# Kernel tuning notes

Measured on AMD Instinct MI355X. Metric: run time of the kernel, lower is better.

Reference implementation:

```python
import jax, jax.numpy as jnp
import numpy as np
from jax import lax

B, T, D_IN, D_H, D_OUT = 64, 512, 256, 1024, 256


def setup_inputs() -> dict:
    key = jax.random.key(0)
    k1, k2, k3, k4 = jax.random.split(key, 4)
    # lecun_normal-style scaling: std = 1/sqrt(fan_in)
    inputs = jax.random.normal(k1, (B, T, D_IN), dtype=jnp.float32)
    input_kernel = jax.random.normal(k2, (D_IN, D_H), dtype=jnp.float32) / np.sqrt(D_IN)
    hidden_kernel = jax.random.normal(k3, (D_H, D_H), dtype=jnp.float32) / np.sqrt(D_H)
    hidden_bias = jnp.zeros((D_H,), dtype=jnp.float32)
    output_kernel = jax.random.normal(k4, (D_H, D_OUT), dtype=jnp.float32) / np.sqrt(D_H)
    output_bias = jnp.zeros((D_OUT,), dtype=jnp.float32)
    return {
        "inputs": inputs,
        "input_kernel": input_kernel,
        "hidden_kernel": hidden_kernel,
        "hidden_bias": hidden_bias,
        "output_kernel": output_kernel,
        "output_bias": output_bias,
    }


def reference(inputs, input_kernel, hidden_kernel, hidden_bias, output_kernel, output_bias):
    # inputs: [B, T, D_in]. Precompute the input projection for all timesteps
    # (batched GEMM) — same math as per-step x_t @ W_in inside scan.
    x_proj = jnp.einsum("bti,ih->bth", inputs, input_kernel) + hidden_bias  # [B,T,H]
    x_proj_tm = jnp.swapaxes(x_proj, 0, 1)  # time-major [T,B,H]

    def step(h, xp_t):
        h_new = jnp.tanh(xp_t + jnp.dot(h, hidden_kernel))  # [B,H]
        return h_new, h_new

    h0 = jnp.zeros((inputs.shape[0], hidden_kernel.shape[0]), dtype=inputs.dtype)
    _, hidden_states = lax.scan(step, h0, x_proj_tm)  # [T,B,H]
    hidden_states = jnp.swapaxes(hidden_states, 0, 1)  # [B,T,H]
    # Dense readout applied to every timestep (return_sequences=True)
    outputs = jnp.einsum("bth,ho->bto", hidden_states, output_kernel) + output_bias
    return outputs
```

## Files before the change

### kernel.cpp

```cpp
#include <hip/hip_runtime.h>
#include <stdint.h>
#include <stddef.h>


#define TT 512
#define HH 1024

typedef __attribute__((ext_vector_type(8))) short short8;
typedef __attribute__((ext_vector_type(4))) float f32x4;
typedef unsigned long long u64;

#define POISON 0xAAAAAAAAAAAAAAAAull

__device__ inline short f2bf(float f) {
  uint32_t u = __builtin_bit_cast(uint32_t, f);
  u += 0x7fffu + ((u >> 16) & 1u);
  return (short)(u >> 16);
}

__device__ inline float fast_tanh(float x) {
  float ax = fabsf(x);
  float e = __expf(-2.f * ax);
  float r = (1.f - e) * __builtin_amdgcn_rcpf(1.f + e);
  return copysignf(r, x);
}

__global__ __launch_bounds__(256, 1) void xproj_kernel(
    const float* __restrict__ inp,
    const float* __restrict__ w_in,
    const float* __restrict__ h_b,
    float* __restrict__ xp) {
  const int blk = blockIdx.x;
  const int c = blk & 3, s = blk >> 2;
  const int tid = threadIdx.x;
  const int wv = tid >> 6, l = tid & 63, lr = l & 15, lq = l >> 4;

  __shared__ short ldsA[16 * 264];

  short8 wf[8][4];
#pragma unroll
  for (int kt = 0; kt < 8; ++kt)
#pragma unroll
    for (int nt = 0; nt < 4; ++nt) {
      int col = c * 256 + (wv * 4 + nt) * 16 + lr;
      int k0 = kt * 32 + lq * 8;
      short8 v;
#pragma unroll
      for (int e = 0; e < 8; ++e) v[e] = f2bf(w_in[(size_t)(k0 + e) * HH + col]);
      wf[kt][nt] = v;
    }
  float bias[4];
#pragma unroll
  for (int nt = 0; nt < 4; ++nt) bias[nt] = h_b[c * 256 + (wv * 4 + nt) * 16 + lr];

  for (int it = 0; it < 32; ++it) {
    int m = s + 64 * it;
    int t = m >> 2, g = m & 3;
    {
      int row = tid >> 4, cb = (tid & 15) * 16;
      const float* src = inp + ((size_t)(g * 16 + row) * TT + t) * 256 + cb;
      f32x4 v0 = *(const f32x4*)(src);
      f32x4 v1 = *(const f32x4*)(src + 4);
      f32x4 v2 = *(const f32x4*)(src + 8);
      f32x4 v3 = *(const f32x4*)(src + 12);
      short8 sa, sb;
      sa[0]=f2bf(v0[0]); sa[1]=f2bf(v0[1]); sa[2]=f2bf(v0[2]); sa[3]=f2bf(v0[3]);
      sa[4]=f2bf(v1[0]); sa[5]=f2bf(v1[1]); sa[6]=f2bf(v1[2]); sa[7]=f2bf(v1[3]);
      sb[0]=f2bf(v2[0]); sb[1]=f2bf(v2[1]); sb[2]=f2bf(v2[2]); sb[3]=f2bf(v2[3]);
      sb[4]=f2bf(v3[0]); sb[5]=f2bf(v3[1]); sb[6]=f2bf(v3[2]); sb[7]=f2bf(v3[3]);
      *(short8*)&ldsA[row * 264 + cb] = sa;
      *(short8*)&ldsA[row * 264 + cb + 8] = sb;
    }
    __syncthreads();

    f32x4 acc[4];
#pragma unroll
    for (int nt = 0; nt < 4; ++nt) acc[nt] = (f32x4){0.f, 0.f, 0.f, 0.f};
#pragma unroll
    for (int kt = 0; kt < 8; ++kt) {
      short8 a = *(const short8*)&ldsA[lr * 264 + kt * 32 + lq * 8];
#pragma unroll
      for (int nt = 0; nt < 4; ++nt)
        acc[nt] = __builtin_amdgcn_mfma_f32_16x16x32_bf16(a, wf[kt][nt], acc[nt], 0, 0, 0);
    }
#pragma unroll
    for (int nt = 0; nt < 4; ++nt) {
      f32x4 o;
#pragma unroll
      for (int i2 = 0; i2 < 4; ++i2) o[i2] = acc[nt][i2] + bias[nt];
      *(f32x4*)(xp + ((size_t)(t * 4 + g) * 64 + c * 16 + wv * 4 + nt) * 256 + l * 4) = o;
    }
    __syncthreads();
  }
}

__global__ __launch_bounds__(256, 1) void scan_kernel(
    const float* __restrict__ xp, const float* __restrict__ w_h,
    short* __restrict__ hbuf) {
  const int blk = blockIdx.x;
  const int g = blk & 3, j = blk >> 2;
  const int tid = threadIdx.x;
  const int wv = tid >> 6, l = tid & 63, lr = l & 15, lq = l >> 4;
  const int ntg = j * 4 + wv;

  __shared__ f32x4 red[4][4][64];
  __shared__ short tr[16][72];

  short8 wf[8][4];
#pragma unroll
  for (int f = 0; f < 8; ++f)
#pragma unroll
    for (int nt = 0; nt < 4; ++nt) {
      int n = j * 64 + nt * 16 + lr;
      int k0 = wv * 256 + f * 32 + lq * 8;
      short8 v;
#pragma unroll
      for (int e = 0; e < 8; ++e) v[e] = f2bf(w_h[(size_t)(k0 + e) * HH + n]);
      wf[f][nt] = v;
    }

  const u64* hq = (const u64*)hbuf;
  u64* hqw = (u64*)hbuf;

  for (int t = 0; t < TT; ++t) {
    f32x4 xpv = *(const f32x4*)(xp + ((size_t)(t * 4 + g) * 64 + ntg) * 256 + l * 4);

    f32x4 acc[4];
#pragma unroll
    for (int nt = 0; nt < 4; ++nt) acc[nt] = (f32x4){0.f, 0.f, 0.f, 0.f};

    if (t > 0) {
      u64 q[16];
      size_t base = (((size_t)((t - 1) * 4 + g) * 32 + wv * 8) * 64 + l) * 2;
      int bad;
      do {
#pragma unroll
        for (int f = 0; f < 8; ++f) {
          q[2 * f]     = __hip_atomic_load(hq + base + (size_t)f * 128,
                                           __ATOMIC_RELAXED, __HIP_MEMORY_SCOPE_AGENT);
          q[2 * f + 1] = __hip_atomic_load(hq + base + (size_t)f * 128 + 1,
                                           __ATOMIC_RELAXED, __HIP_MEMORY_SCOPE_AGENT);
        }
        int mybad = 0;
#pragma unroll
        for (int i = 0; i < 16; ++i) mybad |= (q[i] == POISON);
        bad = __any(mybad);
      } while (bad);

      short8 af[8];
#pragma unroll
      for (int f = 0; f < 8; ++f) {
        union { u64 qq[2]; short8 s; } u;
        u.qq[0] = q[2 * f];
        u.qq[1] = q[2 * f + 1];
        af[f] = u.s;
      }
#pragma unroll
      for (int f = 0; f < 8; ++f)
#pragma unroll
        for (int nt = 0; nt < 4; ++nt)
          acc[nt] = __builtin_amdgcn_mfma_f32_16x16x32_bf16(af[f], wf[f][nt], acc[nt], 0, 0, 0);
    }

    red[wv][0][l] = acc[0];
    red[wv][1][l] = acc[1];
    red[wv][2][l] = acc[2];
    red[wv][3][l] = acc[3];
    __syncthreads();
    f32x4 tot = red[0][wv][l] + red[1][wv][l] + red[2][wv][l] + red[3][wv][l];

#pragma unroll
    for (int i2 = 0; i2 < 4; ++i2) {
      float v = tot[i2] + xpv[i2];
      tr[lq * 4 + i2][wv * 16 + lr] = f2bf(fast_tanh(v));
    }
    __syncthreads();

    if (wv < 2) {
      short8 hv = *(const short8*)&tr[lr][wv * 32 + lq * 8];
      union { short8 s; u64 qq[2]; } u;
      u.s = hv;
      size_t wbase = (((size_t)(t * 4 + g) * 32 + (j * 2 + wv)) * 64 + l) * 2;
      __hip_atomic_store(hqw + wbase, u.qq[0],
                         __ATOMIC_RELAXED, __HIP_MEMORY_SCOPE_AGENT);
      __hip_atomic_store(hqw + wbase + 1, u.qq[1],
                         __ATOMIC_RELAXED, __HIP_MEMORY_SCOPE_AGENT);
    }
  }
}

__global__ __launch_bounds__(256, 1) void outproj_kernel(
    const short* __restrict__ hbuf, const float* __restrict__ w_o,
    const float* __restrict__ o_b, float* __restrict__ out) {
  const int blk = blockIdx.x;
  const int c = blk & 3, s = blk >> 2;
  const int tid = threadIdx.x;
  const int wv = tid >> 6, l = tid & 63, lr = l & 15, lq = l >> 4;

  __shared__ f32x4 red[4][4][64];

  short8 wf[8][4];
#pragma unroll
  for (int f = 0; f < 8; ++f)
#pragma unroll
    for (int nt = 0; nt < 4; ++nt) {
      int o = c * 64 + nt * 16 + lr;
      int k0 = wv * 256 + f * 32 + lq * 8;
      short8 v;
#pragma unroll
      for (int e = 0; e < 8; ++e) v[e] = f2bf(w_o[(size_t)(k0 + e) * 256 + o]);
      wf[f][nt] = v;
    }
  float bias = o_b[c * 64 + wv * 16 + lr];
  const short8* hfr = (const short8*)hbuf;

  for (int it = 0; it < 32; ++it) {
    int m = s + 64 * it;
    int t = m >> 2, g = m & 3;
    short8 af[8];
    size_t base = ((size_t)(t * 4 + g) * 32 + wv * 8) * 64 + l;
#pragma unroll
    for (int f = 0; f < 8; ++f) af[f] = hfr[base + (size_t)f * 64];
    f32x4 acc[4];
#pragma unroll
    for (int nt = 0; nt < 4; ++nt) acc[nt] = (f32x4){0.f, 0.f, 0.f, 0.f};
#pragma unroll
    for (int f = 0; f < 8; ++f)
#pragma unroll
      for (int nt = 0; nt < 4; ++nt)
        acc[nt] = __builtin_amdgcn_mfma_f32_16x16x32_bf16(af[f], wf[f][nt], acc[nt], 0, 0, 0);

    red[wv][0][l] = acc[0];
    red[wv][1][l] = acc[1];
    red[wv][2][l] = acc[2];
    red[wv][3][l] = acc[3];
    __syncthreads();
    f32x4 tot = red[0][wv][l] + red[1][wv][l] + red[2][wv][l] + red[3][wv][l];
#pragma unroll
    for (int i2 = 0; i2 < 4; ++i2) {
      int b = g * 16 + lq * 4 + i2;
      out[((size_t)b * TT + t) * 256 + c * 64 + wv * 16 + lr] = tot[i2] + bias;
    }
    __syncthreads();
  }
}

extern "C" void kernel_launch(void* const* d_in, const int* in_sizes, int n_in,
                              void* d_out, int out_size, void* d_ws, size_t ws_size,
                              hipStream_t stream) {
  const float* inp  = (const float*)d_in[0];
  const float* w_in = (const float*)d_in[1];
  const float* w_h  = (const float*)d_in[2];
  const float* h_b  = (const float*)d_in[3];
  const float* w_o  = (const float*)d_in[4];
  const float* o_b  = (const float*)d_in[5];

  float* xp   = (float*)d_ws;
  short* hbuf = (short*)((char*)d_ws + (size_t)134217728);

  xproj_kernel<<<256, 256, 0, stream>>>(inp, w_in, h_b, xp);
  scan_kernel<<<64, 256, 0, stream>>>(xp, w_h, hbuf);
  outproj_kernel<<<256, 256, 0, stream>>>(hbuf, w_o, o_b, (float*)d_out);
}
```

Baseline: 1.389 ms.

## Fuse input projection, scan, and readout into one concurrently running kernel

Merges the three kernels into one launch. 64 blocks run the recurrent scan while 192 other blocks compute the input projection and then the output projection. Blocks hand data to each other by polling for the POISON sentinel in the workspace, so the scan can start before the whole input projection is done and the readout overlaps with the scan. The risks are that this relies on every block being resident at the same time (otherwise it deadlocks), that producer blocks compete with the latency-critical scan blocks for resources, and that the constant polling adds memory traffic.

```diff
diff --git a/kernel.cpp b/kernel.cpp
--- a/kernel.cpp
+++ b/kernel.cpp
@@ -12,236 +12,276 @@
 
 #define POISON 0xAAAAAAAAAAAAAAAAull
 
-__device__ inline short f2bf(float f) {
+__device__ __forceinline__ short f2bf(float f) {
   uint32_t u = __builtin_bit_cast(uint32_t, f);
   u += 0x7fffu + ((u >> 16) & 1u);
   return (short)(u >> 16);
 }
 
-__device__ inline float fast_tanh(float x) {
+__device__ __forceinline__ float fast_tanh(float x) {
   float ax = fabsf(x);
   float e = __expf(-2.f * ax);
   float r = (1.f - e) * __builtin_amdgcn_rcpf(1.f + e);
   return copysignf(r, x);
 }
 
-__global__ __launch_bounds__(256, 1) void xproj_kernel(
-    const float* __restrict__ inp,
-    const float* __restrict__ w_in,
-    const float* __restrict__ h_b,
-    float* __restrict__ xp) {
+__device__ __forceinline__ u64 ald(const u64* p) {
+  return __hip_atomic_load(p, __ATOMIC_RELAXED, __HIP_MEMORY_SCOPE_AGENT);
+}
+__device__ __forceinline__ void ast(u64* p, u64 v) {
+  __hip_atomic_store(p, v, __ATOMIC_RELAXED, __HIP_MEMORY_SCOPE_AGENT);
+}
+
+__global__ __launch_bounds__(256, 2) void rnn_fused(
+    const float* __restrict__ inp, const float* __restrict__ w_in,
+    const float* __restrict__ w_h, const float* __restrict__ h_b,
+    const float* __restrict__ w_o, const float* __restrict__ o_b,
+    float* __restrict__ xp, short* __restrict__ hbuf,
+    float* __restrict__ out) {
+  __shared__ __attribute__((aligned(16))) char smem[18688];
   const int blk = blockIdx.x;
-  const int c = blk & 3, s = blk >> 2;
   const int tid = threadIdx.x;
   const int wv = tid >> 6, l = tid & 63, lr = l & 15, lq = l >> 4;
 
-  __shared__ short ldsA[16 * 264];
-
-  short8 wf[8][4];
-#pragma unroll
-  for (int kt = 0; kt < 8; ++kt)
-#pragma unroll
-    for (int nt = 0; nt < 4; ++nt) {
-      int col = c * 256 + (wv * 4 + nt) * 16 + lr;
-      int k0 = kt * 32 + lq * 8;
-      short8 v;
-#pragma unroll
-      for (int e = 0; e < 8; ++e) v[e] = f2bf(w_in[(size_t)(k0 + e) * HH + col]);
-      wf[kt][nt] = v;
+  if (blk < 64) {
+    const int g = blk & 3, j = blk >> 2;
+    const int ntg = j * 4 + wv;
+
+    f32x4 (*red)[4][64] = (f32x4 (*)[4][64])smem;
+    short (*tr)[72] = (short (*)[72])(smem + 16384);
+
+    short8 wf[8][4];
+#pragma unroll
+    for (int f = 0; f < 8; ++f)
+#pragma unroll
+      for (int nt = 0; nt < 4; ++nt) {
+        int n = j * 64 + nt * 16 + lr;
+        int k0 = wv * 256 + f * 32 + lq * 8;
+        short8 v;
+#pragma unroll
+        for (int e = 0; e < 8; ++e) v[e] = f2bf(w_h[(size_t)(k0 + e) * HH + n]);
+        wf[f][nt] = v;
+      }
+
+    const u64* hq = (const u64*)hbuf;
+    u64* hqw = (u64*)hbuf;
+    const u64* xq = (const u64*)xp;
+
+    for (int t = 0; t < TT; ++t) {
+      size_t xb = ((size_t)(t * 4 + g) * 64 + ntg) * 128 + (size_t)l * 2;
+      u64 x0 = ald(xq + xb), x1 = ald(xq + xb + 1);
+
+      f32x4 acc[4];
+#pragma unroll
+      for (int nt = 0; nt < 4; ++nt) acc[nt] = (f32x4){0.f, 0.f, 0.f, 0.f};
+
+      if (t > 0) {
+        u64 q[16];
+        size_t base = (((size_t)((t - 1) * 4 + g) * 32 + wv * 8) * 64 + l) * 2;
+        int bad;
+        do {
+#pragma unroll
+          for (int f = 0; f < 8; ++f) {
+            q[2 * f]     = ald(hq + base + (size_t)f * 128);
+            q[2 * f + 1] = ald(hq + base + (size_t)f * 128 + 1);
+          }
+          int mybad = 0;
+#pragma unroll
+          for (int i = 0; i < 16; ++i) mybad |= (q[i] == POISON);
+          bad = __any(mybad);
+        } while (bad);
+
+        short8 af[8];
+#pragma unroll
+        for (int f = 0; f < 8; ++f) {
+          union { u64 qq[2]; short8 s; } u;
+          u.qq[0] = q[2 * f];
+          u.qq[1] = q[2 * f + 1];
+          af[f] = u.s;
+        }
+#pragma unroll
+        for (int f = 0; f < 8; ++f)
+#pragma unroll
+          for (int nt = 0; nt < 4; ++nt)
+            acc[nt] = __builtin_amdgcn_mfma_f32_16x16x32_bf16(af[f], wf[f][nt], acc[nt], 0, 0, 0);
+      }
+
+      red[wv][0][l] = acc[0];
+      red[wv][1][l] = acc[1];
+      red[wv][2][l] = acc[2];
+      red[wv][3][l] = acc[3];
+      __syncthreads();
+      f32x4 tot = red[0][wv][l] + red[1][wv][l] + red[2][wv][l] + red[3][wv][l];
+
+      while (__any((x0 == POISON) | (x1 == POISON))) {
+        x0 = ald(xq + xb);
+        x1 = ald(xq + xb + 1);
+      }
+      union { u64 qq[2]; f32x4 v; } xu;
+      xu.qq[0] = x0;
+      xu.qq[1] = x1;
+
+#pragma unroll
+      for (int i2 = 0; i2 < 4; ++i2) {
+        float v = tot[i2] + xu.v[i2];
+        tr[lq * 4 + i2][wv * 16 + lr] = f2bf(fast_tanh(v));
+      }
+      __syncthreads();
+
+      if (wv < 2) {
+        short8 hv = *(const short8*)&tr[lr][wv * 32 + lq * 8];
+        union { short8 s; u64 qq[2]; } u;
+        u.s = hv;
+        size_t wbase = (((size_t)(t * 4 + g) * 32 + (j * 2 + wv)) * 64 + l) * 2;
+        ast(hqw + wbase, u.qq[0]);
+        ast(hqw + wbase + 1, u.qq[1]);
+      }
     }
-  float bias[4];
-#pragma unroll
-  for (int nt = 0; nt < 4; ++nt) bias[nt] = h_b[c * 256 + (wv * 4 + nt) * 16 + lr];
-
-  for (int it = 0; it < 32; ++it) {
-    int m = s + 64 * it;
-    int t = m >> 2, g = m & 3;
+  } else {
+    const int w = blk - 64;
+    const int c = w & 3, s48 = w >> 2;
+
     {
-      int row = tid >> 4, cb = (tid & 15) * 16;
-      const float* src = inp + ((size_t)(g * 16 + row) * TT + t) * 256 + cb;
-      f32x4 v0 = *(const f32x4*)(src);
-      f32x4 v1 = *(const f32x4*)(src + 4);
-      f32x4 v2 = *(const f32x4*)(src + 8);
-      f32x4 v3 = *(const f32x4*)(src + 12);
-      short8 sa, sb;
-      sa[0]=f2bf(v0[0]); sa[1]=f2bf(v0[1]); sa[2]=f2bf(v0[2]); sa[3]=f2bf(v0[3]);
-      sa[4]=f2bf(v1[0]); sa[5]=f2bf(v1[1]); sa[6]=f2bf(v1[2]); sa[7]=f2bf(v1[3]);
-      sb[0]=f2bf(v2[0]); sb[1]=f2bf(v2[1]); sb[2]=f2bf(v2[2]); sb[3]=f2bf(v2[3]);
-      sb[4]=f2bf(v3[0]); sb[5]=f2bf(v3[1]); sb[6]=f2bf(v3[2]); sb[7]=f2bf(v3[3]);
-      *(short8*)&ldsA[row * 264 + cb] = sa;
-      *(short8*)&ldsA[row * 264 + cb + 8] = sb;
+      short* ldsA = (short*)smem;
+
+      short8 wfx[8][4];
+#pragma unroll
+      for (int kt = 0; kt < 8; ++kt)
+#pragma unroll
+        for (int nt = 0; nt < 4; ++nt) {
+          int col = c * 256 + (wv * 4 + nt) * 16 + lr;
+          int k0 = kt * 32 + lq * 8;
+          short8 v;
+#pragma unroll
+          for (int e = 0; e < 8; ++e) v[e] = f2bf(w_in[(size_t)(k0 + e) * HH + col]);
+          wfx[kt][nt] = v;
+        }
+      float bias[4];
+#pragma unroll
+      for (int nt = 0; nt < 4; ++nt) bias[nt] = h_b[c * 256 + (wv * 4 + nt) * 16 + lr];
+
+      u64* xqw = (u64*)xp;
+      for (int k = 0; k < 43; ++k) {
+        int m = s48 + 48 * k;
+        if (m >= 2048) break;
+        int t = m >> 2, g2 = m & 3;
+        {
+          int row = tid >> 4, cb = (tid & 15) * 16;
+          const float* src = inp + ((size_t)(g2 * 16 + row) * TT + t) * 256 + cb;
+          f32x4 v0 = *(const f32x4*)(src);
+          f32x4 v1 = *(const f32x4*)(src + 4);
+          f32x4 v2 = *(const f32x4*)(src + 8);
+          f32x4 v3 = *(const f32x4*)(src + 12);
+          short8 sa, sb;
+          sa[0]=f2bf(v0[0]); sa[1]=f2bf(v0[1]); sa[2]=f2bf(v0[2]); sa[3]=f2bf(v0[3]);
+          sa[4]=f2bf(v1[0]); sa[5]=f2bf(v1[1]); sa[6]=f2bf(v1[2]); sa[7]=f2bf(v1[3]);
+          sb[0]=f2bf(v2[0]); sb[1]=f2bf(v2[1]); sb[2]=f2bf(v2[2]); sb[3]=f2bf(v2[3]);
+          sb[4]=f2bf(v3[0]); sb[5]=f2bf(v3[1]); sb[6]=f2bf(v3[2]); sb[7]=f2bf(v3[3]);
+          *(short8*)&ldsA[row * 264 + cb] = sa;
+          *(short8*)&ldsA[row * 264 + cb + 8] = sb;
+        }
+        __syncthreads();
+
+        f32x4 acc[4];
+#pragma unroll
+        for (int nt = 0; nt < 4; ++nt) acc[nt] = (f32x4){0.f, 0.f, 0.f, 0.f};
+#pragma unroll
+        for (int kt = 0; kt < 8; ++kt) {
+          short8 a = *(const short8*)&ldsA[lr * 264 + kt * 32 + lq * 8];
+#pragma unroll
+          for (int nt = 0; nt < 4; ++nt)
+            acc[nt] = __builtin_amdgcn_mfma_f32_16x16x32_bf16(a, wfx[kt][nt], acc[nt], 0, 0, 0);
+        }
+#pragma unroll
+        for (int nt = 0; nt < 4; ++nt) {
+          union { f32x4 v; u64 qq[2]; } u;
+#pragma unroll
+          for (int i2 = 0; i2 < 4; ++i2) u.v[i2] = acc[nt][i2] + bias[nt];
+          size_t base =
+              ((size_t)(t * 4 + g2) * 64 + c * 16 + wv * 4 + nt) * 128 + (size_t)l * 2;
+          ast(xqw + base, u.qq[0]);
+          ast(xqw + base + 1, u.qq[1]);
+        }
+        __syncthreads();
+      }
     }
-    __syncthreads();
-
-    f32x4 acc[4];
-#pragma unroll
-    for (int nt = 0; nt < 4; ++nt) acc[nt] = (f32x4){0.f, 0.f, 0.f, 0.f};
-#pragma unroll
-    for (int kt = 0; kt < 8; ++kt) {
-      short8 a = *(const short8*)&ldsA[lr * 264 + kt * 32 + lq * 8];
-#pragma unroll
-      for (int nt = 0; nt < 4; ++nt)
-        acc[nt] = __builtin_amdgcn_mfma_f32_16x16x32_bf16(a, wf[kt][nt], acc[nt], 0, 0, 0);
+
+    {
+      f32x4 (*red)[4][64] = (f32x4 (*)[4][64])smem;
+
+      short8 wfo[8][4];
+#pragma unroll
+      for (int f = 0; f < 8; ++f)
+#pragma unroll
+        for (int nt = 0; nt < 4; ++nt) {
+          int o = c * 64 + nt * 16 + lr;
+          int k0 = wv * 256 + f * 32 + lq * 8;
+          short8 v;
+#pragma unroll
+          for (int e = 0; e < 8; ++e) v[e] = f2bf(w_o[(size_t)(k0 + e) * 256 + o]);
+          wfo[f][nt] = v;
+        }
+      float bias = o_b[c * 64 + wv * 16 + lr];
+      const u64* hq = (const u64*)hbuf;
+
+      for (int k = 0; k < 43; ++k) {
+        int m = s48 + 48 * k;
+        if (m >= 2048) break;
+        int t = m >> 2, g2 = m & 3;
+
+        u64 q[16];
+        size_t base = (((size_t)(t * 4 + g2) * 32 + wv * 8) * 64 + l) * 2;
+        for (;;) {
+          q[0] = ald(hq + base);
+          q[1] = ald(hq + base + 1);
+          if (!__any((q[0] == POISON) | (q[1] == POISON))) break;
+          __builtin_amdgcn_s_sleep(32);
+        }
+        int bad;
+        do {
+#pragma unroll
+          for (int f = 1; f < 8; ++f) {
+            q[2 * f]     = ald(hq + base + (size_t)f * 128);
+            q[2 * f + 1] = ald(hq + base + (size_t)f * 128 + 1);
+          }
+          int mybad = 0;
+#pragma unroll
+          for (int i = 2; i < 16; ++i) mybad |= (q[i] == POISON);
+          bad = __any(mybad);
+          if (bad) __builtin_amdgcn_s_sleep(8);
+        } while (bad);
+
+        short8 af[8];
+#pragma unroll
+        for (int f = 0; f < 8; ++f) {
+          union { u64 qq[2]; short8 s; } u;
+          u.qq[0] = q[2 * f];
+          u.qq[1] = q[2 * f + 1];
+          af[f] = u.s;
+        }
+        f32x4 acc[4];
+#pragma unroll
+        for (int nt = 0; nt < 4; ++nt) acc[nt] = (f32x4){0.f, 0.f, 0.f, 0.f};
+#pragma unroll
+        for (int f = 0; f < 8; ++f)
+#pragma unroll
+          for (int nt = 0; nt < 4; ++nt)
+            acc[nt] = __builtin_amdgcn_mfma_f32_16x16x32_bf16(af[f], wfo[f][nt], acc[nt], 0, 0, 0);
+
+        red[wv][0][l] = acc[0];
+        red[wv][1][l] = acc[1];
+        red[wv][2][l] = acc[2];
+        red[wv][3][l] = acc[3];
+        __syncthreads();
+        f32x4 tot = red[0][wv][l] + red[1][wv][l] + red[2][wv][l] + red[3][wv][l];
+#pragma unroll
+        for (int i2 = 0; i2 < 4; ++i2) {
+          int b = g2 * 16 + lq * 4 + i2;
+          out[((size_t)b * TT + t) * 256 + c * 64 + wv * 16 + lr] = tot[i2] + bias;
+        }
+        __syncthreads();
+      }
     }
-#pragma unroll
-    for (int nt = 0; nt < 4; ++nt) {
-      f32x4 o;
-#pragma unroll
-      for (int i2 = 0; i2 < 4; ++i2) o[i2] = acc[nt][i2] + bias[nt];
-      *(f32x4*)(xp + ((size_t)(t * 4 + g) * 64 + c * 16 + wv * 4 + nt) * 256 + l * 4) = o;
-    }
-    __syncthreads();
-  }
-}
-
-__global__ __launch_bounds__(256, 1) void scan_kernel(
-    const float* __restrict__ xp, const float* __restrict__ w_h,
-    short* __restrict__ hbuf) {
-  const int blk = blockIdx.x;
-  const int g = blk & 3, j = blk >> 2;
-  const int tid = threadIdx.x;
-  const int wv = tid >> 6, l = tid & 63, lr = l & 15, lq = l >> 4;
-  const int ntg = j * 4 + wv;
-
-  __shared__ f32x4 red[4][4][64];
-  __shared__ short tr[16][72];
-
-  short8 wf[8][4];
-#pragma unroll
-  for (int f = 0; f < 8; ++f)
-#pragma unroll
-    for (int nt = 0; nt < 4; ++nt) {
-      int n = j * 64 + nt * 16 + lr;
-      int k0 = wv * 256 + f * 32 + lq * 8;
-      short8 v;
-#pragma unroll
-      for (int e = 0; e < 8; ++e) v[e] = f2bf(w_h[(size_t)(k0 + e) * HH + n]);
-      wf[f][nt] = v;
-    }
-
-  const u64* hq = (const u64*)hbuf;
-  u64* hqw = (u64*)hbuf;
-
-  for (int t = 0; t < TT; ++t) {
-    f32x4 xpv = *(const f32x4*)(xp + ((size_t)(t * 4 + g) * 64 + ntg) * 256 + l * 4);
-
-    f32x4 acc[4];
-#pragma unroll
-    for (int nt = 0; nt < 4; ++nt) acc[nt] = (f32x4){0.f, 0.f, 0.f, 0.f};
-
-    if (t > 0) {
-      u64 q[16];
-      size_t base = (((size_t)((t - 1) * 4 + g) * 32 + wv * 8) * 64 + l) * 2;
-      int bad;
-      do {
-#pragma unroll
-        for (int f = 0; f < 8; ++f) {
-          q[2 * f]     = __hip_atomic_load(hq + base + (size_t)f * 128,
-                                           __ATOMIC_RELAXED, __HIP_MEMORY_SCOPE_AGENT);
-          q[2 * f + 1] = __hip_atomic_load(hq + base + (size_t)f * 128 + 1,
-                                           __ATOMIC_RELAXED, __HIP_MEMORY_SCOPE_AGENT);
-        }
-        int mybad = 0;
-#pragma unroll
-        for (int i = 0; i < 16; ++i) mybad |= (q[i] == POISON);
-        bad = __any(mybad);
-      } while (bad);
-
-      short8 af[8];
-#pragma unroll
-      for (int f = 0; f < 8; ++f) {
-        union { u64 qq[2]; short8 s; } u;
-        u.qq[0] = q[2 * f];
-        u.qq[1] = q[2 * f + 1];
-        af[f] = u.s;
-      }
-#pragma unroll
-      for (int f = 0; f < 8; ++f)
-#pragma unroll
-        for (int nt = 0; nt < 4; ++nt)
-          acc[nt] = __builtin_amdgcn_mfma_f32_16x16x32_bf16(af[f], wf[f][nt], acc[nt], 0, 0, 0);
-    }
-
-    red[wv][0][l] = acc[0];
-    red[wv][1][l] = acc[1];
-    red[wv][2][l] = acc[2];
-    red[wv][3][l] = acc[3];
-    __syncthreads();
-    f32x4 tot = red[0][wv][l] + red[1][wv][l] + red[2][wv][l] + red[3][wv][l];
-
-#pragma unroll
-    for (int i2 = 0; i2 < 4; ++i2) {
-      float v = tot[i2] + xpv[i2];
-      tr[lq * 4 + i2][wv * 16 + lr] = f2bf(fast_tanh(v));
-    }
-    __syncthreads();
-
-    if (wv < 2) {
-      short8 hv = *(const short8*)&tr[lr][wv * 32 + lq * 8];
-      union { short8 s; u64 qq[2]; } u;
-      u.s = hv;
-      size_t wbase = (((size_t)(t * 4 + g) * 32 + (j * 2 + wv)) * 64 + l) * 2;
-      __hip_atomic_store(hqw + wbase, u.qq[0],
-                         __ATOMIC_RELAXED, __HIP_MEMORY_SCOPE_AGENT);
-      __hip_atomic_store(hqw + wbase + 1, u.qq[1],
-                         __ATOMIC_RELAXED, __HIP_MEMORY_SCOPE_AGENT);
-    }
-  }
-}
-
-__global__ __launch_bounds__(256, 1) void outproj_kernel(
-    const short* __restrict__ hbuf, const float* __restrict__ w_o,
-    const float* __restrict__ o_b, float* __restrict__ out) {
-  const int blk = blockIdx.x;
-  const int c = blk & 3, s = blk >> 2;
-  const int tid = threadIdx.x;
-  const int wv = tid >> 6, l = tid & 63, lr = l & 15, lq = l >> 4;
-
-  __shared__ f32x4 red[4][4][64];
-
-  short8 wf[8][4];
-#pragma unroll
-  for (int f = 0; f < 8; ++f)
-#pragma unroll
-    for (int nt = 0; nt < 4; ++nt) {
-      int o = c * 64 + nt * 16 + lr;
-      int k0 = wv * 256 + f * 32 + lq * 8;
-      short8 v;
-#pragma unroll
-      for (int e = 0; e < 8; ++e) v[e] = f2bf(w_o[(size_t)(k0 + e) * 256 + o]);
-      wf[f][nt] = v;
-    }
-  float bias = o_b[c * 64 + wv * 16 + lr];
-  const short8* hfr = (const short8*)hbuf;
-
-  for (int it = 0; it < 32; ++it) {
-    int m = s + 64 * it;
-    int t = m >> 2, g = m & 3;
-    short8 af[8];
-    size_t base = ((size_t)(t * 4 + g) * 32 + wv * 8) * 64 + l;
-#pragma unroll
-    for (int f = 0; f < 8; ++f) af[f] = hfr[base + (size_t)f * 64];
-    f32x4 acc[4];
-#pragma unroll
-    for (int nt = 0; nt < 4; ++nt) acc[nt] = (f32x4){0.f, 0.f, 0.f, 0.f};
-#pragma unroll
-    for (int f = 0; f < 8; ++f)
-#pragma unroll
-      for (int nt = 0; nt < 4; ++nt)
-        acc[nt] = __builtin_amdgcn_mfma_f32_16x16x32_bf16(af[f], wf[f][nt], acc[nt], 0, 0, 0);
-
-    red[wv][0][l] = acc[0];
-    red[wv][1][l] = acc[1];
-    red[wv][2][l] = acc[2];
-    red[wv][3][l] = acc[3];
-    __syncthreads();
-    f32x4 tot = red[0][wv][l] + red[1][wv][l] + red[2][wv][l] + red[3][wv][l];
-#pragma unroll
-    for (int i2 = 0; i2 < 4; ++i2) {
-      int b = g * 16 + lq * 4 + i2;
-      out[((size_t)b * TT + t) * 256 + c * 64 + wv * 16 + lr] = tot[i2] + bias;
-    }
-    __syncthreads();
   }
 }
 
@@ -258,7 +298,6 @@
   float* xp   = (float*)d_ws;
   short* hbuf = (short*)((char*)d_ws + (size_t)134217728);
 
-  xproj_kernel<<<256, 256, 0, stream>>>(inp, w_in, h_b, xp);
-  scan_kernel<<<64, 256, 0, stream>>>(xp, w_h, hbuf);
-  outproj_kernel<<<256, 256, 0, stream>>>(hbuf, w_o, o_b, (float*)d_out);
-}
+  rnn_fused<<<256, 256, 0, stream>>>(inp, w_in, w_h, h_b, w_o, o_b, xp, hbuf,
+                                     (float*)d_out);
+}
```

New measurement: 1.248 ms, median of 2. 10.1% less time.
